# Performance work log

Hardware: AMD Instinct MI355X
Metric: run time of the kernel (lower is better)

## Reference

```python
import jax, jax.numpy as jnp
import numpy as np

N, IN_F, OUT_F, K = 256, 8192, 8320, 16
J = OUT_F - IN_F  # 128


def setup_inputs() -> dict:
    key = jax.random.key(0)
    k1, k2 = jax.random.split(key)
    tensor = jax.random.normal(k1, (N, IN_F), dtype=jnp.float32)
    T = jax.random.normal(k2, (IN_F, J, K), dtype=jnp.float32)
    return {"tensor": tensor, "T": T}


def reference(tensor, T):
    # flatten(start_dim=1) is identity for rank-2 input
    x = tensor.reshape(tensor.shape[0], -1)            # [N, IN_F]
    feats = jnp.einsum('ni,ijk->njk', x, T)            # [N, J, K]
    # pairwise L1 across batch: [N,1,J,K] - [N,J,K] -> [N,N,J,K]
    diff = jnp.abs(feats[:, None, :, :] - feats[None, :, :, :])
    l1 = jnp.sum(diff, axis=3)                         # [N, N, J]
    diversity = jnp.sum(jnp.exp(-l1), axis=1)          # [N, J]
    return jnp.concatenate((x, diversity), axis=1)     # [N, IN_F + J]
```

## Files before the change

### kernel.cpp

```cpp
#include <hip/hip_runtime.h>

typedef unsigned int  u32;
typedef unsigned short u16;

typedef __bf16 bf16x8 __attribute__((ext_vector_type(8)));
typedef float  floatx4 __attribute__((ext_vector_type(4)));

#define N_ROWS 256
#define IN_F   8192
#define OUT_F  8320
#define JDIM   128
#define KDIM   16
#define JK     2048

#define BN     64
#define BK     32
#define KCHUNK 512

typedef const __attribute__((address_space(1))) u32 gu32;
typedef __attribute__((address_space(3))) u32 su32;

__device__ __forceinline__ u16 f2bf(float f) {
    u32 u = __float_as_uint(f);
    u32 r = u + 0x7fffu + ((u >> 16) & 1u);
    return (u16)(r >> 16);
}

__global__ __launch_bounds__(256) void prep_kernel(const float* __restrict__ X,
                                                   float* __restrict__ out,
                                                   u16* __restrict__ Xb,
                                                   float* __restrict__ feats)
{
    int t = blockIdx.x * 256 + threadIdx.x;
    float4 v = reinterpret_cast<const float4*>(X)[t];
    int row = t >> 11;
    int c4  = t & 2047;
    reinterpret_cast<float4*>(out + (size_t)row * OUT_F)[c4] = v;
    ushort4 b;
    b.x = f2bf(v.x); b.y = f2bf(v.y); b.z = f2bf(v.z); b.w = f2bf(v.w);
    reinterpret_cast<ushort4*>(Xb)[t] = b;
    if (t < 131072) reinterpret_cast<float4*>(feats)[t] = make_float4(0.f, 0.f, 0.f, 0.f);
    if (t < 8192) {
        int r2 = t >> 5, j4 = t & 31;
        reinterpret_cast<float4*>(out + (size_t)r2 * OUT_F + IN_F)[j4] = make_float4(0.f, 0.f, 0.f, 0.f);
    }
}

__global__ __launch_bounds__(256) void gemm_kernel(const u16* __restrict__ Xb,
                                                   const float* __restrict__ W,
                                                   float* __restrict__ feats)
{
    __shared__ u16 xs[N_ROWS * BK];
    __shared__ u16 wt[BN * 40];

    const int tid  = threadIdx.x;
    const int lane = tid & 63;
    const int wave = tid >> 6;
    const int c0   = blockIdx.x * BN;
    const int kbase = blockIdx.y * KCHUNK;

    floatx4 acc[4][4] = {};

    const int xrow_in_grp = lane >> 2;
    const int xqs         = lane & 3;
    const int wc  = tid >> 2;
    const int wkp = tid & 3;

    for (int kk = 0; kk < KCHUNK; kk += BK) {
        const int k0 = kbase + kk;
        __syncthreads();

        #pragma unroll
        for (int g = 0; g < 4; ++g) {
            int row = wave * 64 + g * 16 + xrow_in_grp;
            int qg  = xqs ^ ((row >> 1) & 3);
            const u16* gp = Xb + (size_t)row * IN_F + k0 + qg * 8;
            u32* lp = (u32*)&xs[(wave * 64 + g * 16) * BK];
            __builtin_amdgcn_global_load_lds((gu32*)gp, (su32*)lp, 16, 0, 0);
        }

        #pragma unroll
        for (int r = 0; r < 4; ++r) {
            int k = r * 8 + wkp * 2;
            const float* wp = W + (size_t)(k0 + k) * JK + c0 + wc;
            float w0 = wp[0];
            float w1 = wp[JK];
            u32 pk = (u32)f2bf(w0) | ((u32)f2bf(w1) << 16);
            *(u32*)&wt[wc * 40 + k] = pk;
        }
        __syncthreads();

        const int q    = lane >> 4;
        const int mrow = lane & 15;
        const int qsw  = q ^ ((mrow >> 1) & 3);
        bf16x8 a[4], b[4];
        #pragma unroll
        for (int rt = 0; rt < 4; ++rt) {
            int row = wave * 64 + rt * 16 + mrow;
            a[rt] = *reinterpret_cast<const bf16x8*>(&xs[row * BK + qsw * 8]);
        }
        #pragma unroll
        for (int ct = 0; ct < 4; ++ct) {
            int col = ct * 16 + mrow;
            b[ct] = *reinterpret_cast<const bf16x8*>(&wt[col * 40 + q * 8]);
        }
        #pragma unroll
        for (int rt = 0; rt < 4; ++rt)
            #pragma unroll
            for (int ct = 0; ct < 4; ++ct)
                acc[rt][ct] = __builtin_amdgcn_mfma_f32_16x16x32_bf16(a[rt], b[ct], acc[rt][ct], 0, 0, 0);
    }

    const int q = lane >> 4;
    const int col_l = lane & 15;
    #pragma unroll
    for (int rt = 0; rt < 4; ++rt)
        #pragma unroll
        for (int ct = 0; ct < 4; ++ct)
            #pragma unroll
            for (int r = 0; r < 4; ++r) {
                int row = wave * 64 + rt * 16 + q * 4 + r;
                int col = c0 + ct * 16 + col_l;
                atomicAdd(&feats[(size_t)row * JK + col], acc[rt][ct][r]);
            }
}

__global__ __launch_bounds__(256) void pairwise_kernel(const float* __restrict__ feats,
                                                       float* __restrict__ out)
{
    const int j = blockIdx.x;
    const int mq = blockIdx.y;
    const int n = threadIdx.x;

    __shared__ float F[N_ROWS * KDIM];
    const float* fr = feats + (size_t)n * JK + j * KDIM;
    float4 v0 = ((const float4*)fr)[0];
    float4 v1 = ((const float4*)fr)[1];
    float4 v2 = ((const float4*)fr)[2];
    float4 v3 = ((const float4*)fr)[3];
    float4* Fp = (float4*)&F[n * KDIM];
    Fp[0] = v0; Fp[1] = v1; Fp[2] = v2; Fp[3] = v3;
    __syncthreads();

    float f[16] = { v0.x, v0.y, v0.z, v0.w, v1.x, v1.y, v1.z, v1.w,
                    v2.x, v2.y, v2.z, v2.w, v3.x, v3.y, v3.z, v3.w };
    float accum = 0.f;
    const int m0 = mq * 64;
    for (int m = 0; m < 64; ++m) {
        const float* Fm = &F[(m0 + m) * KDIM];
        float l1 = 0.f;
        #pragma unroll
        for (int k = 0; k < 16; ++k) l1 += fabsf(f[k] - Fm[k]);
        accum += exp2f(-1.4426950408889634f * l1);
    }
    atomicAdd(&out[(size_t)n * OUT_F + IN_F + j], accum);
}

extern "C" void kernel_launch(void* const* d_in, const int* in_sizes, int n_in,
                              void* d_out, int out_size, void* d_ws, size_t ws_size,
                              hipStream_t stream)
{
    const float* X = (const float*)d_in[0];
    const float* T = (const float*)d_in[1];
    float* out = (float*)d_out;

    float* feats = (float*)d_ws;
    u16*   Xb    = (u16*)((char*)d_ws + 2u * 1024 * 1024);

    prep_kernel<<<2048, 256, 0, stream>>>(X, out, Xb, feats);
    gemm_kernel<<<dim3(JK / BN, IN_F / KCHUNK), 256, 0, stream>>>(Xb, T, feats);
    pairwise_kernel<<<dim3(JDIM, 4), 256, 0, stream>>>(feats, out);
}
```

Baseline: 158.4 us.

## Replace atomic split-K GEMM with bf16 partial slabs and separate reduction

The GEMM now splits the 256 rows into two 128-row tiles and uses BK=64 with XOR-swizzled LDS for both operands. Split-K partials are written as bf16 slabs instead of being accumulated with float atomics, and a new reduce kernel sums them into feats. This removes the atomic contention and the zeroing of feats, and raises block count and occupancy. In exchange it adds slab write/read traffic, an extra kernel launch, and rounds partial sums to bf16, which loses precision.

```diff
diff --git a/kernel.cpp b/kernel.cpp
--- a/kernel.cpp
+++ b/kernel.cpp
@@ -13,23 +13,22 @@
 #define KDIM   16
 #define JK     2048
 
+#define BM     128
 #define BN     64
-#define BK     32
-#define KCHUNK 512
+#define BK     64
 
 typedef const __attribute__((address_space(1))) u32 gu32;
 typedef __attribute__((address_space(3))) u32 su32;
 
 __device__ __forceinline__ u16 f2bf(float f) {
     u32 u = __float_as_uint(f);
-    u32 r = u + 0x7fffu + ((u >> 16) & 1u);
-    return (u16)(r >> 16);
-}
+    return (u16)((u + 0x7fffu + ((u >> 16) & 1u)) >> 16);
+}
+__device__ __forceinline__ float bf2f(u16 h) { return __uint_as_float(((u32)h) << 16); }
 
 __global__ __launch_bounds__(256) void prep_kernel(const float* __restrict__ X,
                                                    float* __restrict__ out,
-                                                   u16* __restrict__ Xb,
-                                                   float* __restrict__ feats)
+                                                   u16* __restrict__ Xb)
 {
     int t = blockIdx.x * 256 + threadIdx.x;
     float4 v = reinterpret_cast<const float4*>(X)[t];
@@ -39,90 +38,122 @@
     ushort4 b;
     b.x = f2bf(v.x); b.y = f2bf(v.y); b.z = f2bf(v.z); b.w = f2bf(v.w);
     reinterpret_cast<ushort4*>(Xb)[t] = b;
-    if (t < 131072) reinterpret_cast<float4*>(feats)[t] = make_float4(0.f, 0.f, 0.f, 0.f);
     if (t < 8192) {
         int r2 = t >> 5, j4 = t & 31;
         reinterpret_cast<float4*>(out + (size_t)r2 * OUT_F + IN_F)[j4] = make_float4(0.f, 0.f, 0.f, 0.f);
     }
 }
 
-__global__ __launch_bounds__(256) void gemm_kernel(const u16* __restrict__ Xb,
-                                                   const float* __restrict__ W,
-                                                   float* __restrict__ feats)
-{
-    __shared__ u16 xs[N_ROWS * BK];
-    __shared__ u16 wt[BN * 40];
+__global__ __launch_bounds__(256, 4) void gemm_kernel(const u16* __restrict__ Xb,
+                                                      const float* __restrict__ W,
+                                                      u16* __restrict__ slabs,
+                                                      int kchunk)
+{
+    __shared__ u16 xs[BM * BK];
+    __shared__ u16 wt[BN * BK];
 
     const int tid  = threadIdx.x;
     const int lane = tid & 63;
     const int wave = tid >> 6;
     const int c0   = blockIdx.x * BN;
-    const int kbase = blockIdx.y * KCHUNK;
-
-    floatx4 acc[4][4] = {};
-
-    const int xrow_in_grp = lane >> 2;
-    const int xqs         = lane & 3;
-    const int wc  = tid >> 2;
-    const int wkp = tid & 3;
-
-    for (int kk = 0; kk < KCHUNK; kk += BK) {
-        const int k0 = kbase + kk;
+    const int row0 = blockIdx.y * BM;
+    const int s    = blockIdx.z;
+    const int k0base = s * kchunk;
+
+    floatx4 acc[2][4] = {};
+
+    const int xrl = lane >> 3;
+    const int xgc = (lane & 7) ^ xrl;
+    const int wcol = lane;
+    const int wkh  = wave;
+
+    const int iters = kchunk >> 6;
+    for (int it = 0; it < iters; ++it) {
+        const int k0 = k0base + it * BK;
         __syncthreads();
 
         #pragma unroll
         for (int g = 0; g < 4; ++g) {
-            int row = wave * 64 + g * 16 + xrow_in_grp;
-            int qg  = xqs ^ ((row >> 1) & 3);
-            const u16* gp = Xb + (size_t)row * IN_F + k0 + qg * 8;
-            u32* lp = (u32*)&xs[(wave * 64 + g * 16) * BK];
+            int rbase = wave * 32 + g * 8;
+            const u16* gp = Xb + (size_t)(row0 + rbase + xrl) * IN_F + k0 + xgc * 8;
+            u32* lp = (u32*)&xs[rbase * BK];
             __builtin_amdgcn_global_load_lds((gu32*)gp, (su32*)lp, 16, 0, 0);
         }
 
-        #pragma unroll
-        for (int r = 0; r < 4; ++r) {
-            int k = r * 8 + wkp * 2;
-            const float* wp = W + (size_t)(k0 + k) * JK + c0 + wc;
-            float w0 = wp[0];
-            float w1 = wp[JK];
-            u32 pk = (u32)f2bf(w0) | ((u32)f2bf(w1) << 16);
-            *(u32*)&wt[wc * 40 + k] = pk;
+        u32 pk[2][4];
+        #pragma unroll
+        for (int cc = 0; cc < 2; ++cc) {
+            int chunk = wkh * 2 + cc;
+            const float* wp = W + (size_t)(k0 + chunk * 8) * JK + c0 + wcol;
+            #pragma unroll
+            for (int p = 0; p < 4; ++p) {
+                float w0 = wp[(size_t)(2 * p) * JK];
+                float w1 = wp[(size_t)(2 * p + 1) * JK];
+                pk[cc][p] = (u32)f2bf(w0) | ((u32)f2bf(w1) << 16);
+            }
+        }
+        #pragma unroll
+        for (int cc = 0; cc < 2; ++cc) {
+            int chunk = wkh * 2 + cc;
+            int slot  = chunk ^ (wcol & 7);
+            *(uint4*)&wt[wcol * BK + slot * 8] = *(uint4*)pk[cc];
         }
         __syncthreads();
 
+        const int mrow = lane & 15;
         const int q    = lane >> 4;
-        const int mrow = lane & 15;
-        const int qsw  = q ^ ((mrow >> 1) & 3);
-        bf16x8 a[4], b[4];
-        #pragma unroll
-        for (int rt = 0; rt < 4; ++rt) {
-            int row = wave * 64 + rt * 16 + mrow;
-            a[rt] = *reinterpret_cast<const bf16x8*>(&xs[row * BK + qsw * 8]);
-        }
-        #pragma unroll
-        for (int ct = 0; ct < 4; ++ct) {
-            int col = ct * 16 + mrow;
-            b[ct] = *reinterpret_cast<const bf16x8*>(&wt[col * 40 + q * 8]);
-        }
-        #pragma unroll
-        for (int rt = 0; rt < 4; ++rt)
-            #pragma unroll
-            for (int ct = 0; ct < 4; ++ct)
-                acc[rt][ct] = __builtin_amdgcn_mfma_f32_16x16x32_bf16(a[rt], b[ct], acc[rt][ct], 0, 0, 0);
-    }
-
-    const int q = lane >> 4;
-    const int col_l = lane & 15;
+        #pragma unroll
+        for (int h = 0; h < 2; ++h) {
+            bf16x8 a[2], b[4];
+            #pragma unroll
+            for (int rt = 0; rt < 2; ++rt) {
+                int rl   = wave * 32 + rt * 16 + mrow;
+                int slot = (h * 4 + q) ^ (rl & 7);
+                a[rt] = *reinterpret_cast<const bf16x8*>(&xs[rl * BK + slot * 8]);
+            }
+            #pragma unroll
+            for (int ct = 0; ct < 4; ++ct) {
+                int col  = ct * 16 + mrow;
+                int slot = (h * 4 + q) ^ (col & 7);
+                b[ct] = *reinterpret_cast<const bf16x8*>(&wt[col * BK + slot * 8]);
+            }
+            #pragma unroll
+            for (int rt = 0; rt < 2; ++rt)
+                #pragma unroll
+                for (int ct = 0; ct < 4; ++ct)
+                    acc[rt][ct] = __builtin_amdgcn_mfma_f32_16x16x32_bf16(a[rt], b[ct], acc[rt][ct], 0, 0, 0);
+        }
+    }
+
+    const int qe = lane >> 4;
+    const int cl = lane & 15;
+    u16* sp = slabs + (size_t)s * N_ROWS * JK;
     #pragma unroll
-    for (int rt = 0; rt < 4; ++rt)
+    for (int rt = 0; rt < 2; ++rt)
         #pragma unroll
         for (int ct = 0; ct < 4; ++ct)
             #pragma unroll
             for (int r = 0; r < 4; ++r) {
-                int row = wave * 64 + rt * 16 + q * 4 + r;
-                int col = c0 + ct * 16 + col_l;
-                atomicAdd(&feats[(size_t)row * JK + col], acc[rt][ct][r]);
-            }
+                int row = row0 + wave * 32 + rt * 16 + qe * 4 + r;
+                int col = c0 + ct * 16 + cl;
+                sp[(size_t)row * JK + col] = f2bf(acc[rt][ct][r]);
+            }
+}
+
+__global__ __launch_bounds__(256) void reduce_kernel(const u16* __restrict__ slabs,
+                                                     float* __restrict__ feats, int S)
+{
+    int t = blockIdx.x * 256 + threadIdx.x;
+    float acc[8] = {};
+    for (int s = 0; s < S; ++s) {
+        uint4 v = *(const uint4*)(slabs + (size_t)s * N_ROWS * JK + (size_t)t * 8);
+        const u16* h = (const u16*)&v;
+        #pragma unroll
+        for (int e = 0; e < 8; ++e) acc[e] += bf2f(h[e]);
+    }
+    float4* fp = (float4*)(feats + (size_t)t * 8);
+    fp[0] = make_float4(acc[0], acc[1], acc[2], acc[3]);
+    fp[1] = make_float4(acc[4], acc[5], acc[6], acc[7]);
 }
 
 __global__ __launch_bounds__(256) void pairwise_kernel(const float* __restrict__ feats,
@@ -165,9 +196,16 @@
     float* out = (float*)d_out;
 
     float* feats = (float*)d_ws;
-    u16*   Xb    = (u16*)((char*)d_ws + 2u * 1024 * 1024);
-
-    prep_kernel<<<2048, 256, 0, stream>>>(X, out, Xb, feats);
-    gemm_kernel<<<dim3(JK / BN, IN_F / KCHUNK), 256, 0, stream>>>(Xb, T, feats);
+    u16*   Xb    = (u16*)((char*)d_ws + (2u << 20));
+    u16*   slabs = (u16*)((char*)d_ws + (6u << 20));
+
+    int S = 16;
+    if (ws_size < (6u << 20) + (size_t)16 * N_ROWS * JK * 2) S = 8;
+    if (ws_size < (6u << 20) + (size_t)8  * N_ROWS * JK * 2) S = 4;
+    int kchunk = IN_F / S;
+
+    prep_kernel<<<2048, 256, 0, stream>>>(X, out, Xb);
+    gemm_kernel<<<dim3(JK / BN, N_ROWS / BM, S), 256, 0, stream>>>(Xb, T, slabs, kchunk);
+    reduce_kernel<<<256, 256, 0, stream>>>(slabs, feats, S);
     pairwise_kernel<<<dim3(JDIM, 4), 256, 0, stream>>>(feats, out);
 }
```

Result: faster. 148.4 us (-6.3%).
